# Kernel tuning notes

Hardware: AMD Instinct MI355X
Metric: run time of the kernel (lower is better)

The kernel has to match this reference:

```python
import jax, jax.numpy as jnp
import numpy as np

N = 2048        # reservoir_size
D_IN = 32       # input_dim
D_OUT = 16      # output_dim
H = 128         # PhysicsEncoder hidden_dim
B, T = 64, 256
LEAK = 0.3
CONNECTIVITY = 0.1
SPECTRAL_RADIUS = 0.95
LN_EPS = 1e-5


def setup_inputs() -> dict:
    key = jax.random.key(0)
    ks = jax.random.split(key, 24)
    x = jax.random.normal(ks[0], (B, T, D_IN), dtype=jnp.float32)
    # frozen input weights, input_scaling = 1.0
    W_in = jax.random.normal(ks[1], (N, D_IN), dtype=jnp.float32)
    # sparse reservoir, rescaled to spectral radius ~0.95 (analytic approx
    # rho ~ sigma*sqrt(N*p) for sparse gaussian, matches the torch rescale intent)
    mask = (jax.random.uniform(ks[2], (N, N)) < CONNECTIVITY).astype(jnp.float32)
    W_res = jax.random.normal(ks[3], (N, N), dtype=jnp.float32) * 0.1 * mask
    approx_radius = 0.1 * np.sqrt(N * CONNECTIVITY)
    W_res = W_res * (SPECTRAL_RADIUS / approx_radius)
    # attention: seq_len is always 1 inside the loop, so softmax over a length-1
    # axis is identically 1 and out == proj(v). Only the V slice of qkv matters.
    sc = 1.0 / np.sqrt(N)
    Wv = jax.random.uniform(ks[4], (N, N), minval=-sc, maxval=sc, dtype=jnp.float32)
    bv = jax.random.uniform(ks[5], (N,), minval=-sc, maxval=sc, dtype=jnp.float32)
    Wproj = jax.random.uniform(ks[6], (N, N), minval=-sc, maxval=sc, dtype=jnp.float32)
    bproj = jax.random.uniform(ks[7], (N,), minval=-sc, maxval=sc, dtype=jnp.float32)
    # physics encoder: Linear(N,H) -> LayerNorm -> GELU -> Linear(H,H) -> GELU -> Linear(H,N)
    s1 = 1.0 / np.sqrt(N)
    We1 = jax.random.uniform(ks[8], (H, N), minval=-s1, maxval=s1, dtype=jnp.float32)
    be1 = jax.random.uniform(ks[9], (H,), minval=-s1, maxval=s1, dtype=jnp.float32)
    ln_g = jnp.ones((H,), jnp.float32)
    ln_b = jnp.zeros((H,), jnp.float32)
    s2 = 1.0 / np.sqrt(H)
    We2 = jax.random.uniform(ks[10], (H, H), minval=-s2, maxval=s2, dtype=jnp.float32)
    be2 = jax.random.uniform(ks[11], (H,), minval=-s2, maxval=s2, dtype=jnp.float32)
    We3 = jax.random.uniform(ks[12], (N, H), minval=-s2, maxval=s2, dtype=jnp.float32)
    be3 = jax.random.uniform(ks[13], (N,), minval=-s2, maxval=s2, dtype=jnp.float32)
    # Bayesian output layer (reparameterized; epsilons passed in for determinism)
    s3 = 1.0 / np.sqrt(N)
    w_mu = jax.random.uniform(ks[14], (D_OUT, N), minval=-s3, maxval=s3, dtype=jnp.float32)
    w_rho = jnp.full((D_OUT, N), -3.0, jnp.float32)
    b_mu = jax.random.uniform(ks[15], (D_OUT,), minval=-s3, maxval=s3, dtype=jnp.float32)
    b_rho = jnp.full((D_OUT,), -3.0, jnp.float32)
    w_eps = jax.random.normal(ks[16], (D_OUT, N), dtype=jnp.float32)
    b_eps = jax.random.normal(ks[17], (D_OUT,), dtype=jnp.float32)
    return {
        "x": x, "W_in": W_in, "W_res": W_res,
        "Wv": Wv, "bv": bv, "Wproj": Wproj, "bproj": bproj,
        "We1": We1, "be1": be1, "ln_g": ln_g, "ln_b": ln_b,
        "We2": We2, "be2": be2, "We3": We3, "be3": be3,
        "w_mu": w_mu, "w_rho": w_rho, "b_mu": b_mu, "b_rho": b_rho,
        "w_eps": w_eps, "b_eps": b_eps,
    }


def _gelu(x):
    return jax.nn.gelu(x, approximate=False)  # torch nn.GELU default = exact erf


def reference(x, W_in, W_res, Wv, bv, Wproj, bproj,
              We1, be1, ln_g, ln_b, We2, be2, We3, be3,
              w_mu, w_rho, b_mu, b_rho, w_eps, b_eps):
    Bsz = x.shape[0]

    def step(states, x_t):
        # terms computed from PRE-attention state, as in the original loop order
        input_term = x_t @ W_in.T            # [B, N]
        reservoir_term = states @ W_res.T    # [B, N]
        # attention over a length-1 sequence: softmax == 1 -> out = proj(v)
        v = states @ Wv.T + bv
        s_att = v @ Wproj.T + bproj          # new `states` after attention
        # physics encoder on attended state
        h = s_att @ We1.T + be1
        mu = jnp.mean(h, axis=-1, keepdims=True)
        var = jnp.var(h, axis=-1, keepdims=True)
        h = (h - mu) * jax.lax.rsqrt(var + LN_EPS) * ln_g + ln_b
        h = _gelu(h)
        h = _gelu(h @ We2.T + be2)
        phys = h @ We3.T + be3               # [B, N]
        new_state = (1.0 - LEAK) * s_att + LEAK * jnp.tanh(
            input_term + reservoir_term + phys)
        return new_state, None

    s0 = jnp.zeros((Bsz, N), x.dtype)
    final_state, _ = jax.lax.scan(step, s0, jnp.swapaxes(x, 0, 1))  # scan over T

    # Bayesian output layer (reparameterization with fixed eps)
    w_sigma = jnp.log1p(jnp.exp(w_rho))
    b_sigma = jnp.log1p(jnp.exp(b_rho))
    weight = w_mu + w_sigma * w_eps
    bias = b_mu + b_sigma * b_eps
    predictions = final_state @ weight.T + bias  # [B, D_OUT]
    return predictions
```

## Files before the change

kernel.cpp:

```cpp
#include <hip/hip_runtime.h>
#include <hip/hip_fp16.h>
#include <cstdint>
#include <cstddef>

typedef _Float16 f16x8 __attribute__((ext_vector_type(8)));
typedef float    f32x4 __attribute__((ext_vector_type(4)));

#define MFMA(A,B,C) __builtin_amdgcn_mfma_f32_16x16x32_f16((A),(B),(C),0,0,0)

#define NRES  2048
#define DIN   32
#define DOUT  16
#define HDIM  128
#define BBATCH 64
#define TSTEPS 256
#define WCOLS 4224
#define NWORK 256
#define NBLK  257

#define OFF_WBIG  ((size_t)0)
#define OFF_WH1   ((size_t)16777216)
#define OFF_BIAS  ((size_t)17301504)
#define OFF_WE2H  ((size_t)17318400)
#define OFF_WE3H  ((size_t)17351168)
#define OFF_S16   ((size_t)17875456)
#define OFF_YP    ((size_t)18137600)
#define OFF_WINH  ((size_t)19219200)
#define OFF_CNT   ((size_t)19350528)

__device__ __forceinline__ float gelu_exact(float v) {
  return 0.5f * v * (1.0f + erff(v * 0.70710678118654752f));
}

__device__ __forceinline__ void stg16(void* p, f32x4 v) {
  asm volatile("global_store_dwordx4 %0, %1, off sc0 sc1" :: "v"(p), "v"(v) : "memory");
}


__global__ void k_cast(const float* __restrict__ src, _Float16* __restrict__ dst, int n) {
  int i = blockIdx.x * blockDim.x + threadIdx.x;
  int stride = gridDim.x * blockDim.x;
  for (; i < n; i += stride) dst[i] = (_Float16)src[i];
}

__global__ void k_batt(const float* __restrict__ Wproj, const float* __restrict__ bv,
                       const float* __restrict__ bproj, float* __restrict__ bias_big) {
  int c = blockIdx.x, tid = threadIdx.x;
  float p = 0.f;
  for (int k = tid; k < NRES; k += 256) p += Wproj[(size_t)c * NRES + k] * bv[k];
  for (int m = 1; m < 64; m <<= 1) p += __shfl_xor(p, m);
  __shared__ float r4[4];
  if ((tid & 63) == 0) r4[tid >> 6] = p;
  __syncthreads();
  if (tid == 0) bias_big[2048 + c] = r4[0] + r4[1] + r4[2] + r4[3] + bproj[c];
}

__global__ void k_bh1(const float* __restrict__ We1, const float* __restrict__ be1,
                      float* __restrict__ bias_big) {
  int h = blockIdx.x, tid = threadIdx.x;
  float p = 0.f;
  for (int n = tid; n < NRES; n += 256) p += We1[(size_t)h * NRES + n] * bias_big[2048 + n];
  for (int m = 1; m < 64; m <<= 1) p += __shfl_xor(p, m);
  __shared__ float r4[4];
  if ((tid & 63) == 0) r4[tid >> 6] = p;
  __syncthreads();
  if (tid == 0) bias_big[4096 + h] = r4[0] + r4[1] + r4[2] + r4[3] + be1[h];
}

__global__ void __launch_bounds__(256) k_gemm1(const float* __restrict__ Wproj,
                                               const float* __restrict__ Wv,
                                               _Float16* __restrict__ wbig) {
  __shared__ _Float16 BT[64][40];
  const int kblock = blockIdx.x, cblock = blockIdx.y;
  const int tid = threadIdx.x, wv = tid >> 6, lane = tid & 63;
  const int l4 = lane >> 4, l15 = lane & 15;
  const int crow0 = cblock * 64 + wv * 16;
  f32x4 acc[4];
  f32x4 zero = {0.f, 0.f, 0.f, 0.f};
  for (int i = 0; i < 4; ++i) acc[i] = zero;

  for (int mc = 0; mc < 64; ++mc) {
    const int m0 = mc * 32;
    {
      int m = tid >> 3, kk = (tid & 7) * 8;
      const float* src = &Wv[(size_t)(m0 + m) * NRES + kblock * 64 + kk];
      float4 v0 = *(const float4*)src;
      float4 v1 = *(const float4*)(src + 4);
      float tmp[8] = {v0.x, v0.y, v0.z, v0.w, v1.x, v1.y, v1.z, v1.w};
      #pragma unroll
      for (int j = 0; j < 8; ++j) BT[kk + j][m] = (_Float16)tmp[j];
    }
    __syncthreads();
    const float* pa = &Wproj[(size_t)(crow0 + l15) * NRES + m0 + l4 * 8];
    float4 a0 = *(const float4*)pa;
    float4 a1 = *(const float4*)(pa + 4);
    f16x8 af;
    af[0]=(_Float16)a0.x; af[1]=(_Float16)a0.y; af[2]=(_Float16)a0.z; af[3]=(_Float16)a0.w;
    af[4]=(_Float16)a1.x; af[5]=(_Float16)a1.y; af[6]=(_Float16)a1.z; af[7]=(_Float16)a1.w;
    #pragma unroll
    for (int kt = 0; kt < 4; ++kt) {
      f16x8 bf = *(const f16x8*)&BT[kt * 16 + l15][l4 * 8];
      acc[kt] = MFMA(af, bf, acc[kt]);
    }
    __syncthreads();
  }
  #pragma unroll
  for (int kt = 0; kt < 4; ++kt)
    #pragma unroll
    for (int i = 0; i < 4; ++i) {
      int c = crow0 + l4 * 4 + i;
      int k = kblock * 64 + kt * 16 + l15;
      wbig[(size_t)(2048 + c) * NRES + k] = (_Float16)acc[kt][i];
    }
}

__global__ void __launch_bounds__(256) k_gemm2(const float* __restrict__ We1,
                                               const _Float16* __restrict__ wbig,
                                               _Float16* __restrict__ wh1) {
  __shared__ _Float16 BT[64][40];
  const int kblock = blockIdx.x, hblock = blockIdx.y;
  const int tid = threadIdx.x, wv = tid >> 6, lane = tid & 63;
  const int l4 = lane >> 4, l15 = lane & 15;
  const int hrow0 = hblock * 64 + wv * 16;
  f32x4 acc[4];
  f32x4 zero = {0.f, 0.f, 0.f, 0.f};
  for (int i = 0; i < 4; ++i) acc[i] = zero;

  for (int nc = 0; nc < 64; ++nc) {
    const int n0 = nc * 32;
    {
      int n = tid >> 3, kk = (tid & 7) * 8;
      f16x8 v = *(const f16x8*)&wbig[(size_t)(2048 + n0 + n) * NRES + kblock * 64 + kk];
      #pragma unroll
      for (int j = 0; j < 8; ++j) BT[kk + j][n] = v[j];
    }
    __syncthreads();
    const float* pa = &We1[(size_t)(hrow0 + l15) * NRES + n0 + l4 * 8];
    float4 a0 = *(const float4*)pa;
    float4 a1 = *(const float4*)(pa + 4);
    f16x8 af;
    af[0]=(_Float16)a0.x; af[1]=(_Float16)a0.y; af[2]=(_Float16)a0.z; af[3]=(_Float16)a0.w;
    af[4]=(_Float16)a1.x; af[5]=(_Float16)a1.y; af[6]=(_Float16)a1.z; af[7]=(_Float16)a1.w;
    #pragma unroll
    for (int kt = 0; kt < 4; ++kt) {
      f16x8 bf = *(const f16x8*)&BT[kt * 16 + l15][l4 * 8];
      acc[kt] = MFMA(af, bf, acc[kt]);
    }
    __syncthreads();
  }
  #pragma unroll
  for (int kt = 0; kt < 4; ++kt)
    #pragma unroll
    for (int i = 0; i < 4; ++i) {
      int h = hrow0 + l4 * 4 + i;
      int k = kblock * 64 + kt * 16 + l15;
      wh1[(size_t)h * NRES + k] = (_Float16)acc[kt][i];
    }
}

__device__ __forceinline__ void gbar3(unsigned* slots, unsigned* wake, int b, unsigned phase) {
  asm volatile("s_waitcnt vmcnt(0)" ::: "memory");
  __syncthreads();
  if (threadIdx.x == 0) {
    __hip_atomic_store(slots + b, phase, __ATOMIC_RELAXED, __HIP_MEMORY_SCOPE_AGENT);
    unsigned spins = 0;
    while (__hip_atomic_load(wake + (size_t)b * 16, __ATOMIC_RELAXED, __HIP_MEMORY_SCOPE_AGENT) < phase) {
      __builtin_amdgcn_s_sleep(1);
      if (++spins > (1u << 20)) break;
    }
    (void)__hip_atomic_load(wake + (size_t)b * 16, __ATOMIC_ACQUIRE, __HIP_MEMORY_SCOPE_AGENT);
  }
  __syncthreads();
}


__global__ void __launch_bounds__(256, 2) k_main(
    const float* __restrict__ x,
    const float* __restrict__ ln_g, const float* __restrict__ ln_b,
    const float* __restrict__ be2v, const float* __restrict__ be3v,
    const float* __restrict__ w_mu, const float* __restrict__ w_rho,
    const float* __restrict__ b_mu, const float* __restrict__ b_rho,
    const float* __restrict__ w_eps, const float* __restrict__ b_eps,
    const _Float16* __restrict__ wbig, const _Float16* __restrict__ wh1,
    const float* __restrict__ bias_big,
    const _Float16* __restrict__ we2h, const _Float16* __restrict__ we3h,
    const _Float16* __restrict__ winh,
    _Float16* s16, float* yp,
    unsigned* cnt, float* __restrict__ out)
{
  const int b = blockIdx.x, tid = threadIdx.x;
  unsigned* slots = cnt;
  unsigned* wake  = cnt + 512;

  if (b == NWORK) {
    if (tid >= 64) return;
    for (unsigned p = 1; p <= 2u * TSTEPS; ++p) {
      unsigned spins = 0;
      for (;;) {
        bool ok = true;
        #pragma unroll
        for (int j = 0; j < 4; ++j) {
          unsigned v = __hip_atomic_load(slots + tid + j * 64, __ATOMIC_RELAXED, __HIP_MEMORY_SCOPE_AGENT);
          ok = ok && (v >= p);
        }
        if (__all((int)ok)) break;
        if (++spins > (1u << 19)) break;
        __builtin_amdgcn_s_sleep(1);
      }
      #pragma unroll
      for (int j = 0; j < 4; ++j)
        __hip_atomic_store(wake + (size_t)(tid + j * 64) * 16, p, __ATOMIC_RELAXED, __HIP_MEMORY_SCOPE_AGENT);
    }
    return;
  }

  const int wv = tid >> 6, lane = tid & 63;
  const int l4 = lane >> 4, l15 = lane & 15;

  __shared__ float    lds_red[4][64][17];
  __shared__ _Float16 lds_w2[128][136];
  __shared__ _Float16 lds_h1[16][136];
  __shared__ _Float16 lds_g2[16][136];
  __shared__ _Float16 lds_x[16][40];
  __shared__ _Float16 lds_ns[16][40];

  const bool dual = (b < 8);
  f16x8 Bf[16];
  #pragma unroll
  for (int ks = 0; ks < 16; ++ks)
    Bf[ks] = *(const f16x8*)&wbig[(size_t)(b * 16 + l15) * NRES + wv * 512 + ks * 32 + l4 * 8];
  const _Float16* wh1p = &wh1[(size_t)(b * 16 + l15) * NRES + wv * 512 + l4 * 8];

  const int R0 = (b >> 6) * 16, C0 = (b & 63) * 32;

  float g8[8], bb8[8], bh8[8];
  #pragma unroll
  for (int jj = 0; jj < 8; ++jj) {
    g8[jj]  = ln_g[l15 + 16 * jj];
    bb8[jj] = ln_b[l15 + 16 * jj];
    bh8[jj] = bias_big[4096 + l15 + 16 * jj];
  }
  float be2r[2];
  #pragma unroll
  for (int ct = 0; ct < 2; ++ct) be2r[ct] = be2v[(wv * 2 + ct) * 16 + l15];

  const int mycol = C0 + wv * 16 + l15;
  f16x8 We3f[4];
  f16x8 Winf;
  float be3r = 0.f, battr = 0.f;
  if (wv < 2) {
    #pragma unroll
    for (int ks = 0; ks < 4; ++ks)
      We3f[ks] = *(const f16x8*)&we3h[(size_t)mycol * HDIM + ks * 32 + l4 * 8];
    be3r  = be3v[mycol];
    battr = bias_big[2048 + mycol];
    Winf  = *(const f16x8*)&winh[(size_t)mycol * DIN + l4 * 8];
  }

  {
    int row = tid >> 1, half = tid & 1;
    #pragma unroll
    for (int j = 0; j < 8; ++j) {
      f16x8 v = *(const f16x8*)&we2h[(size_t)row * HDIM + half * 64 + j * 8];
      *(f16x8*)&lds_w2[row][half * 64 + j * 8] = v;
    }
  }
  __syncthreads();

  const f32x4 zero = {0.f, 0.f, 0.f, 0.f};
  unsigned phase = 0;

  const int cr  = tid >> 2, cch = tid & 3;
  const int rqi = (cr >> 4) * 4 + (cr & 3);
  const int pl4 = (cr >> 2) & 3;

  for (int t = 0; t < TSTEPS; ++t) {
    f32x4 a0 = zero, a1 = zero, a2 = zero, a3 = zero;
    f32x4 e0 = zero, e1 = zero, e2 = zero, e3 = zero;
    #pragma unroll
    for (int ks = 0; ks < 16; ++ks) {
      const int kk = wv * 512 + ks * 32 + l4 * 8;
      f16x8 A0 = *(const f16x8*)&s16[(size_t)(l15) * NRES + kk];
      f16x8 A1 = *(const f16x8*)&s16[(size_t)(16 + l15) * NRES + kk];
      f16x8 A2 = *(const f16x8*)&s16[(size_t)(32 + l15) * NRES + kk];
      f16x8 A3 = *(const f16x8*)&s16[(size_t)(48 + l15) * NRES + kk];
      a0 = MFMA(A0, Bf[ks], a0);
      a1 = MFMA(A1, Bf[ks], a1);
      a2 = MFMA(A2, Bf[ks], a2);
      a3 = MFMA(A3, Bf[ks], a3);
      if (dual) {
        f16x8 Bx = *(const f16x8*)&wh1p[ks * 32];
        e0 = MFMA(A0, Bx, e0);
        e1 = MFMA(A1, Bx, e1);
        e2 = MFMA(A2, Bx, e2);
        e3 = MFMA(A3, Bx, e3);
      }
    }
    #pragma unroll
    for (int i = 0; i < 4; ++i) {
      lds_red[wv][lane][0 + i]  = a0[i];
      lds_red[wv][lane][4 + i]  = a1[i];
      lds_red[wv][lane][8 + i]  = a2[i];
      lds_red[wv][lane][12 + i] = a3[i];
    }
    __syncthreads();
    {
      f32x4 v;
      #pragma unroll
      for (int c = 0; c < 4; ++c) {
        int pl = pl4 * 16 + cch * 4 + c;
        v[c] = lds_red[0][pl][rqi] + lds_red[1][pl][rqi]
             + lds_red[2][pl][rqi] + lds_red[3][pl][rqi];
      }
      stg16(&yp[(size_t)cr * WCOLS + b * 16 + cch * 4], v);
    }
    if (dual) {
      __syncthreads();
      #pragma unroll
      for (int i = 0; i < 4; ++i) {
        lds_red[wv][lane][0 + i]  = e0[i];
        lds_red[wv][lane][4 + i]  = e1[i];
        lds_red[wv][lane][8 + i]  = e2[i];
        lds_red[wv][lane][12 + i] = e3[i];
      }
      __syncthreads();
      f32x4 v2;
      #pragma unroll
      for (int c = 0; c < 4; ++c) {
        int pl = pl4 * 16 + cch * 4 + c;
        v2[c] = lds_red[0][pl][rqi] + lds_red[1][pl][rqi]
              + lds_red[2][pl][rqi] + lds_red[3][pl][rqi];
      }
      stg16(&yp[(size_t)cr * WCOLS + 4096 + b * 16 + cch * 4], v2);
    }
    ++phase;
    gbar3(slots, wake, b, phase);

    {
      int xr = tid >> 4, k0 = (tid & 15) * 2;
      const float* xs = &x[((size_t)(R0 + xr) * TSTEPS + t) * DIN + k0];
      lds_x[xr][k0]     = (_Float16)xs[0];
      lds_x[xr][k0 + 1] = (_Float16)xs[1];
    }
    const int lr = wv * 4 + l4;
    float h1v[8], s1 = 0.f, s2 = 0.f;
    const size_t yb = (size_t)(R0 + lr) * WCOLS + 4096;
    #pragma unroll
    for (int jj = 0; jj < 8; ++jj) {
      float v = yp[yb + l15 + 16 * jj] + bh8[jj];
      h1v[jj] = v; s1 += v; s2 += v * v;
    }
    #pragma unroll
    for (int m = 1; m < 16; m <<= 1) { s1 += __shfl_xor(s1, m); s2 += __shfl_xor(s2, m); }
    const float mu = s1 * (1.f / 128.f);
    const float var = s2 * (1.f / 128.f) - mu * mu;
    const float rs = rsqrtf(var + 1e-5f);
    #pragma unroll
    for (int jj = 0; jj < 8; ++jj) {
      float hn = (h1v[jj] - mu) * rs * g8[jj] + bb8[jj];
      lds_h1[lr][l15 + 16 * jj] = (_Float16)gelu_exact(hn);
    }
    __syncthreads();
    f32x4 c0 = zero, c1 = zero;
    #pragma unroll
    for (int ks = 0; ks < 4; ++ks) {
      f16x8 af = *(const f16x8*)&lds_h1[l15][ks * 32 + l4 * 8];
      f16x8 b0 = *(const f16x8*)&lds_w2[(wv * 2 + 0) * 16 + l15][ks * 32 + l4 * 8];
      f16x8 b1 = *(const f16x8*)&lds_w2[(wv * 2 + 1) * 16 + l15][ks * 32 + l4 * 8];
      c0 = MFMA(af, b0, c0);
      c1 = MFMA(af, b1, c1);
    }
    #pragma unroll
    for (int i = 0; i < 4; ++i) {
      int rr = l4 * 4 + i;
      lds_g2[rr][(wv * 2 + 0) * 16 + l15] = (_Float16)gelu_exact(c0[i] + be2r[0]);
      lds_g2[rr][(wv * 2 + 1) * 16 + l15] = (_Float16)gelu_exact(c1[i] + be2r[1]);
    }
    __syncthreads();
    if (wv < 2) {
      f32x4 accp = zero;
      #pragma unroll
      for (int ks = 0; ks < 4; ++ks) {
        f16x8 af = *(const f16x8*)&lds_g2[l15][ks * 32 + l4 * 8];
        accp = MFMA(af, We3f[ks], accp);
      }
      f16x8 ax = *(const f16x8*)&lds_x[l15][l4 * 8];
      f32x4 acci = MFMA(ax, Winf, zero);
      #pragma unroll
      for (int i = 0; i < 4; ++i) {
        int r2 = l4 * 4 + i;
        float satt = yp[(size_t)(R0 + r2) * WCOLS + 2048 + mycol] + battr;
        float rrv  = yp[(size_t)(R0 + r2) * WCOLS + mycol];
        float ns = 0.7f * satt + 0.3f * tanhf(acci[i] + rrv + accp[i] + be3r);
        lds_ns[r2][wv * 16 + l15] = (_Float16)ns;
      }
    }
    __syncthreads();
    if (tid < 64) {
      int r = tid >> 2, ch = tid & 3;
      f16x8 v = *(const f16x8*)&lds_ns[r][ch * 8];
      stg16(&s16[(size_t)(R0 + r) * NRES + C0 + ch * 8], __builtin_bit_cast(f32x4, v));
    }
    ++phase;
    gbar3(slots, wake, b, phase);
  }

  if (b < BBATCH) {
    float* red = &lds_red[0][0][0];
    int o = tid >> 4, sg = tid & 15;
    float p = 0.f;
    for (int n = sg * 128; n < sg * 128 + 128; ++n) {
      float sv = (float)s16[(size_t)b * NRES + n];
      float w = w_mu[(size_t)o * NRES + n]
              + log1pf(expf(w_rho[(size_t)o * NRES + n])) * w_eps[(size_t)o * NRES + n];
      p += sv * w;
    }
    red[o * 17 + sg] = p;
    __syncthreads();
    if (tid < DOUT) {
      float sum = 0.f;
      for (int q = 0; q < 16; ++q) sum += red[tid * 17 + q];
      float bs = b_mu[tid] + log1pf(expf(b_rho[tid])) * b_eps[tid];
      out[b * DOUT + tid] = sum + bs;
    }
  }
}


extern "C" void kernel_launch(void* const* d_in, const int* in_sizes, int n_in,
                              void* d_out, int out_size, void* d_ws, size_t ws_size,
                              hipStream_t stream) {
  (void)in_sizes; (void)n_in; (void)out_size; (void)ws_size;
  const float* x     = (const float*)d_in[0];
  const float* W_in  = (const float*)d_in[1];
  const float* W_res = (const float*)d_in[2];
  const float* Wv    = (const float*)d_in[3];
  const float* bv    = (const float*)d_in[4];
  const float* Wproj = (const float*)d_in[5];
  const float* bproj = (const float*)d_in[6];
  const float* We1   = (const float*)d_in[7];
  const float* be1   = (const float*)d_in[8];
  const float* ln_g  = (const float*)d_in[9];
  const float* ln_b  = (const float*)d_in[10];
  const float* We2   = (const float*)d_in[11];
  const float* be2   = (const float*)d_in[12];
  const float* We3   = (const float*)d_in[13];
  const float* be3   = (const float*)d_in[14];
  const float* w_mu  = (const float*)d_in[15];
  const float* w_rho = (const float*)d_in[16];
  const float* b_mu  = (const float*)d_in[17];
  const float* b_rho = (const float*)d_in[18];
  const float* w_eps = (const float*)d_in[19];
  const float* b_eps = (const float*)d_in[20];
  float* out = (float*)d_out;

  char* ws = (char*)d_ws;
  _Float16* wbig     = (_Float16*)(ws + OFF_WBIG);
  _Float16* wh1      = (_Float16*)(ws + OFF_WH1);
  float*    bias_big = (float*)(ws + OFF_BIAS);
  _Float16* we2h     = (_Float16*)(ws + OFF_WE2H);
  _Float16* we3h     = (_Float16*)(ws + OFF_WE3H);
  _Float16* s16      = (_Float16*)(ws + OFF_S16);
  float*    yp       = (float*)(ws + OFF_YP);
  _Float16* winh     = (_Float16*)(ws + OFF_WINH);
  unsigned* cnt      = (unsigned*)(ws + OFF_CNT);

  hipMemsetAsync(bias_big, 0, WCOLS * sizeof(float), stream);
  hipMemsetAsync(s16, 0, (size_t)BBATCH * NRES * sizeof(_Float16), stream);
  hipMemsetAsync(cnt, 0, 512 * 4 + 256 * 64, stream);

  k_cast<<<4096, 256, 0, stream>>>(W_res, wbig, NRES * NRES);
  k_cast<<<64,   256, 0, stream>>>(We2, we2h, HDIM * HDIM);
  k_cast<<<1024, 256, 0, stream>>>(We3, we3h, NRES * HDIM);
  k_cast<<<256,  256, 0, stream>>>(W_in, winh, NRES * DIN);
  k_batt<<<NRES, 256, 0, stream>>>(Wproj, bv, bproj, bias_big);
  k_gemm1<<<dim3(32, 32), 256, 0, stream>>>(Wproj, Wv, wbig);
  k_bh1<<<HDIM, 256, 0, stream>>>(We1, be1, bias_big);
  k_gemm2<<<dim3(32, 2), 256, 0, stream>>>(We1, wbig, wh1);

  k_main<<<NBLK, 256, 0, stream>>>(x, ln_g, ln_b, be2, be3,
                                   w_mu, w_rho, b_mu, b_rho, w_eps, b_eps,
                                   wbig, wh1, bias_big, we2h, we3h, winh, s16, yp, cnt, out);
}
```

Measured before the change: 6.630 ms.

## Software-pipeline state loads with cache-bypassing asm and move small weights to LDS

The per-step GEMV now loads the shared state through inline-asm global loads with sc0 sc1 bits, kept in a three-deep register ring with explicit vmcnt waits so loads overlap the MFMAs. The second weight tile (wh1) for the dual blocks is preloaded into registers instead of being re-read from global memory every step. The We3, W_in and layernorm parameters move from registers into LDS, and the acquire load in the barrier is removed, with the explicit coherent loads relied on instead. This aims to hide global latency in the serialized recurrence, at the cost of higher register pressure and memory-ordering subtleties around the removed acquire.

After: 7.984 ms. 1.2x slower.

```diff
diff --git a/kernel.cpp b/kernel.cpp
--- a/kernel.cpp
+++ b/kernel.cpp
@@ -35,6 +35,10 @@
 __device__ __forceinline__ void stg16(void* p, f32x4 v) {
   asm volatile("global_store_dwordx4 %0, %1, off sc0 sc1" :: "v"(p), "v"(v) : "memory");
 }
+#define LDG16(dst, ptr) \
+  asm volatile("global_load_dwordx4 %0, %1, off sc0 sc1" : "=v"(dst) : "v"(ptr) : "memory")
+#define LDGF(dst, ptr) \
+  asm volatile("global_load_dword %0, %1, off sc0 sc1" : "=v"(dst) : "v"(ptr) : "memory")
 
 
 __global__ void k_cast(const float* __restrict__ src, _Float16* __restrict__ dst, int n) {
@@ -168,7 +172,6 @@
       __builtin_amdgcn_s_sleep(1);
       if (++spins > (1u << 20)) break;
     }
-    (void)__hip_atomic_load(wake + (size_t)b * 16, __ATOMIC_ACQUIRE, __HIP_MEMORY_SCOPE_AGENT);
   }
   __syncthreads();
 }
@@ -219,53 +222,64 @@
 
   __shared__ float    lds_red[4][64][17];
   __shared__ _Float16 lds_w2[128][136];
+  __shared__ _Float16 lds_w3[32][136];
+  __shared__ _Float16 lds_wi[32][40];
+  __shared__ float    lds_lnp[3][128];
   __shared__ _Float16 lds_h1[16][136];
   __shared__ _Float16 lds_g2[16][136];
   __shared__ _Float16 lds_x[16][40];
   __shared__ _Float16 lds_ns[16][40];
 
   const bool dual = (b < 8);
-  f16x8 Bf[16];
+  f16x8 Bf[16], Bf2[16];
   #pragma unroll
   for (int ks = 0; ks < 16; ++ks)
     Bf[ks] = *(const f16x8*)&wbig[(size_t)(b * 16 + l15) * NRES + wv * 512 + ks * 32 + l4 * 8];
-  const _Float16* wh1p = &wh1[(size_t)(b * 16 + l15) * NRES + wv * 512 + l4 * 8];
+  if (dual) {
+    #pragma unroll
+    for (int ks = 0; ks < 16; ++ks)
+      Bf2[ks] = *(const f16x8*)&wh1[(size_t)(b * 16 + l15) * NRES + wv * 512 + ks * 32 + l4 * 8];
+  }
 
   const int R0 = (b >> 6) * 16, C0 = (b & 63) * 32;
-
-  float g8[8], bb8[8], bh8[8];
-  #pragma unroll
-  for (int jj = 0; jj < 8; ++jj) {
-    g8[jj]  = ln_g[l15 + 16 * jj];
-    bb8[jj] = ln_b[l15 + 16 * jj];
-    bh8[jj] = bias_big[4096 + l15 + 16 * jj];
-  }
+  const int mycol = C0 + wv * 16 + l15;
+  const int lcol  = wv * 16 + l15;
+
   float be2r[2];
   #pragma unroll
   for (int ct = 0; ct < 2; ++ct) be2r[ct] = be2v[(wv * 2 + ct) * 16 + l15];
-
-  const int mycol = C0 + wv * 16 + l15;
-  f16x8 We3f[4];
-  f16x8 Winf;
   float be3r = 0.f, battr = 0.f;
   if (wv < 2) {
-    #pragma unroll
-    for (int ks = 0; ks < 4; ++ks)
-      We3f[ks] = *(const f16x8*)&we3h[(size_t)mycol * HDIM + ks * 32 + l4 * 8];
     be3r  = be3v[mycol];
     battr = bias_big[2048 + mycol];
-    Winf  = *(const f16x8*)&winh[(size_t)mycol * DIN + l4 * 8];
   }
 
   {
     int row = tid >> 1, half = tid & 1;
     #pragma unroll
-    for (int j = 0; j < 8; ++j) {
-      f16x8 v = *(const f16x8*)&we2h[(size_t)row * HDIM + half * 64 + j * 8];
-      *(f16x8*)&lds_w2[row][half * 64 + j * 8] = v;
+    for (int j = 0; j < 8; ++j)
+      *(f16x8*)&lds_w2[row][half * 64 + j * 8] =
+          *(const f16x8*)&we2h[(size_t)row * HDIM + half * 64 + j * 8];
+    for (int idx = tid; idx < 32 * 16; idx += 256) {
+      int c = idx >> 4, kk8 = (idx & 15) * 8;
+      *(f16x8*)&lds_w3[c][kk8] = *(const f16x8*)&we3h[(size_t)(C0 + c) * HDIM + kk8];
+    }
+    for (int idx = tid; idx < 32 * 4; idx += 256) {
+      int c = idx >> 2, kk8 = (idx & 3) * 8;
+      *(f16x8*)&lds_wi[c][kk8] = *(const f16x8*)&winh[(size_t)(C0 + c) * DIN + kk8];
+    }
+    if (tid < 128) {
+      lds_lnp[0][tid] = ln_g[tid];
+      lds_lnp[1][tid] = ln_b[tid];
+      lds_lnp[2][tid] = bias_big[4096 + tid];
     }
   }
   __syncthreads();
+
+  const _Float16* q0 = s16 + (size_t)(l15) * NRES + wv * 512 + l4 * 8;
+  const _Float16* q1 = q0 + 16 * NRES;
+  const _Float16* q2 = q0 + 32 * NRES;
+  const _Float16* q3 = q0 + 48 * NRES;
 
   const f32x4 zero = {0.f, 0.f, 0.f, 0.f};
   unsigned phase = 0;
@@ -277,23 +291,38 @@
   for (int t = 0; t < TSTEPS; ++t) {
     f32x4 a0 = zero, a1 = zero, a2 = zero, a3 = zero;
     f32x4 e0 = zero, e1 = zero, e2 = zero, e3 = zero;
-    #pragma unroll
-    for (int ks = 0; ks < 16; ++ks) {
-      const int kk = wv * 512 + ks * 32 + l4 * 8;
-      f16x8 A0 = *(const f16x8*)&s16[(size_t)(l15) * NRES + kk];
-      f16x8 A1 = *(const f16x8*)&s16[(size_t)(16 + l15) * NRES + kk];
-      f16x8 A2 = *(const f16x8*)&s16[(size_t)(32 + l15) * NRES + kk];
-      f16x8 A3 = *(const f16x8*)&s16[(size_t)(48 + l15) * NRES + kk];
-      a0 = MFMA(A0, Bf[ks], a0);
-      a1 = MFMA(A1, Bf[ks], a1);
-      a2 = MFMA(A2, Bf[ks], a2);
-      a3 = MFMA(A3, Bf[ks], a3);
-      if (dual) {
-        f16x8 Bx = *(const f16x8*)&wh1p[ks * 32];
-        e0 = MFMA(A0, Bx, e0);
-        e1 = MFMA(A1, Bx, e1);
-        e2 = MFMA(A2, Bx, e2);
-        e3 = MFMA(A3, Bx, e3);
+    {
+      f16x8 A[3][4];
+      #pragma unroll
+      for (int c = 0; c < 3; ++c) {
+        LDG16(A[c][0], q0 + c * 32);
+        LDG16(A[c][1], q1 + c * 32);
+        LDG16(A[c][2], q2 + c * 32);
+        LDG16(A[c][3], q3 + c * 32);
+      }
+      #pragma unroll
+      for (int ks = 0; ks < 16; ++ks) {
+        if (ks <= 13)      { asm volatile("s_waitcnt vmcnt(8)" ::: "memory"); }
+        else if (ks == 14) { asm volatile("s_waitcnt vmcnt(4)" ::: "memory"); }
+        else               { asm volatile("s_waitcnt vmcnt(0)" ::: "memory"); }
+        __builtin_amdgcn_sched_barrier(0);
+        const int sl = ks % 3;
+        a0 = MFMA(A[sl][0], Bf[ks], a0);
+        a1 = MFMA(A[sl][1], Bf[ks], a1);
+        a2 = MFMA(A[sl][2], Bf[ks], a2);
+        a3 = MFMA(A[sl][3], Bf[ks], a3);
+        if (dual) {
+          e0 = MFMA(A[sl][0], Bf2[ks], e0);
+          e1 = MFMA(A[sl][1], Bf2[ks], e1);
+          e2 = MFMA(A[sl][2], Bf2[ks], e2);
+          e3 = MFMA(A[sl][3], Bf2[ks], e3);
+        }
+        if (ks + 3 < 16) {
+          LDG16(A[sl][0], q0 + (ks + 3) * 32);
+          LDG16(A[sl][1], q1 + (ks + 3) * 32);
+          LDG16(A[sl][2], q2 + (ks + 3) * 32);
+          LDG16(A[sl][3], q3 + (ks + 3) * 32);
+        }
       }
     }
     #pragma unroll
@@ -343,11 +372,18 @@
       lds_x[xr][k0 + 1] = (_Float16)xs[1];
     }
     const int lr = wv * 4 + l4;
+    float hv[8];
+    {
+      const float* hp = &yp[(size_t)(R0 + lr) * WCOLS + 4096 + l15];
+      #pragma unroll
+      for (int jj = 0; jj < 8; ++jj) LDGF(hv[jj], hp + 16 * jj);
+      asm volatile("s_waitcnt vmcnt(0)" ::: "memory");
+      __builtin_amdgcn_sched_barrier(0);
+    }
     float h1v[8], s1 = 0.f, s2 = 0.f;
-    const size_t yb = (size_t)(R0 + lr) * WCOLS + 4096;
     #pragma unroll
     for (int jj = 0; jj < 8; ++jj) {
-      float v = yp[yb + l15 + 16 * jj] + bh8[jj];
+      float v = hv[jj] + lds_lnp[2][l15 + 16 * jj];
       h1v[jj] = v; s1 += v; s2 += v * v;
     }
     #pragma unroll
@@ -357,8 +393,9 @@
     const float rs = rsqrtf(var + 1e-5f);
     #pragma unroll
     for (int jj = 0; jj < 8; ++jj) {
-      float hn = (h1v[jj] - mu) * rs * g8[jj] + bb8[jj];
-      lds_h1[lr][l15 + 16 * jj] = (_Float16)gelu_exact(hn);
+      int j = l15 + 16 * jj;
+      float hn = (h1v[jj] - mu) * rs * lds_lnp[0][j] + lds_lnp[1][j];
+      lds_h1[lr][j] = (_Float16)gelu_exact(hn);
     }
     __syncthreads();
     f32x4 c0 = zero, c1 = zero;
@@ -378,20 +415,31 @@
     }
     __syncthreads();
     if (wv < 2) {
+      float sattv[4], rrvv[4];
+      #pragma unroll
+      for (int i = 0; i < 4; ++i) {
+        const float* pa_ = &yp[(size_t)(R0 + l4 * 4 + i) * WCOLS + 2048 + mycol];
+        const float* pb_ = &yp[(size_t)(R0 + l4 * 4 + i) * WCOLS + mycol];
+        LDGF(sattv[i], pa_);
+        LDGF(rrvv[i], pb_);
+      }
       f32x4 accp = zero;
       #pragma unroll
       for (int ks = 0; ks < 4; ++ks) {
         f16x8 af = *(const f16x8*)&lds_g2[l15][ks * 32 + l4 * 8];
-        accp = MFMA(af, We3f[ks], accp);
+        f16x8 w3 = *(const f16x8*)&lds_w3[lcol][ks * 32 + l4 * 8];
+        accp = MFMA(af, w3, accp);
       }
       f16x8 ax = *(const f16x8*)&lds_x[l15][l4 * 8];
-      f32x4 acci = MFMA(ax, Winf, zero);
+      f16x8 wi = *(const f16x8*)&lds_wi[lcol][l4 * 8];
+      f32x4 acci = MFMA(ax, wi, zero);
+      asm volatile("s_waitcnt vmcnt(0)" ::: "memory");
+      __builtin_amdgcn_sched_barrier(0);
       #pragma unroll
       for (int i = 0; i < 4; ++i) {
         int r2 = l4 * 4 + i;
-        float satt = yp[(size_t)(R0 + r2) * WCOLS + 2048 + mycol] + battr;
-        float rrv  = yp[(size_t)(R0 + r2) * WCOLS + mycol];
-        float ns = 0.7f * satt + 0.3f * tanhf(acci[i] + rrv + accp[i] + be3r);
+        float satt = sattv[i] + battr;
+        float ns = 0.7f * satt + 0.3f * tanhf(acci[i] + rrvv[i] + accp[i] + be3r);
         lds_ns[r2][wv * 16 + l15] = (_Float16)ns;
       }
     }
@@ -408,12 +456,25 @@
   if (b < BBATCH) {
     float* red = &lds_red[0][0][0];
     int o = tid >> 4, sg = tid & 15;
+    f16x8 sbuf[16];
+    {
+      const _Float16* sp = &s16[(size_t)b * NRES + sg * 128];
+      #pragma unroll
+      for (int jj = 0; jj < 16; ++jj) LDG16(sbuf[jj], sp + jj * 8);
+      asm volatile("s_waitcnt vmcnt(0)" ::: "memory");
+      __builtin_amdgcn_sched_barrier(0);
+    }
     float p = 0.f;
-    for (int n = sg * 128; n < sg * 128 + 128; ++n) {
-      float sv = (float)s16[(size_t)b * NRES + n];
-      float w = w_mu[(size_t)o * NRES + n]
-              + log1pf(expf(w_rho[(size_t)o * NRES + n])) * w_eps[(size_t)o * NRES + n];
-      p += sv * w;
+    #pragma unroll
+    for (int jj = 0; jj < 16; ++jj) {
+      #pragma unroll
+      for (int k = 0; k < 8; ++k) {
+        int n = sg * 128 + jj * 8 + k;
+        float sv = (float)sbuf[jj][k];
+        float w = w_mu[(size_t)o * NRES + n]
+                + log1pf(expf(w_rho[(size_t)o * NRES + n])) * w_eps[(size_t)o * NRES + n];
+        p += sv * w;
+      }
     }
     red[o * 17 + sg] = p;
     __syncthreads();
```

## Interleave reservoir and attention weight rows to halve grid barriers per step

Applied to the files above, without the earlier changes.

W_res and the fused Wproj·Wv rows are packed so each block's 16 output columns hold 8 reservoir and the matching 8 attention columns. This lets every block finish its own state update locally without the yp global scratch exchange. The encoder first layer moves to 4 dedicated blocks that work on a double-buffered state and signal through per-block flags. The result is one grid barrier per timestep instead of two. The trade-off is that the encoder blocks carry extra serial work that every block must wait on, and half the MFMA output lanes in the final step are wasted.

After: 9.719 ms. +46.6%, slower.

```diff
diff --git a/kernel.cpp b/kernel.cpp
--- a/kernel.cpp
+++ b/kernel.cpp
@@ -14,19 +14,19 @@
 #define HDIM  128
 #define BBATCH 64
 #define TSTEPS 256
-#define WCOLS 4224
 #define NWORK 256
 #define NBLK  257
-
-#define OFF_WBIG  ((size_t)0)
+#define S16N  (BBATCH * NRES)
+
+#define OFF_WPK   ((size_t)0)
 #define OFF_WH1   ((size_t)16777216)
 #define OFF_BIAS  ((size_t)17301504)
 #define OFF_WE2H  ((size_t)17318400)
 #define OFF_WE3H  ((size_t)17351168)
 #define OFF_S16   ((size_t)17875456)
-#define OFF_YP    ((size_t)18137600)
-#define OFF_WINH  ((size_t)19219200)
-#define OFF_CNT   ((size_t)19350528)
+#define OFF_WINH  ((size_t)18399744)
+#define OFF_G2    ((size_t)18530816)
+#define OFF_CNT   ((size_t)18547200)
 
 __device__ __forceinline__ float gelu_exact(float v) {
   return 0.5f * v * (1.0f + erff(v * 0.70710678118654752f));
@@ -41,6 +41,15 @@
   int i = blockIdx.x * blockDim.x + threadIdx.x;
   int stride = gridDim.x * blockDim.x;
   for (; i < n; i += stride) dst[i] = (_Float16)src[i];
+}
+
+__global__ void k_castres(const float* __restrict__ W_res, _Float16* __restrict__ wpk) {
+  int c = blockIdx.x, k0 = threadIdx.x * 8;
+  int pr = (c >> 3) * 16 + (c & 7);
+  const float* s = &W_res[(size_t)c * NRES + k0];
+  _Float16* d = &wpk[(size_t)pr * NRES + k0];
+  #pragma unroll
+  for (int j = 0; j < 8; ++j) d[j] = (_Float16)s[j];
 }
 
 __global__ void k_batt(const float* __restrict__ Wproj, const float* __restrict__ bv,
@@ -69,7 +78,7 @@
 
 __global__ void __launch_bounds__(256) k_gemm1(const float* __restrict__ Wproj,
                                                const float* __restrict__ Wv,
-                                               _Float16* __restrict__ wbig) {
+                                               _Float16* __restrict__ wpk) {
   __shared__ _Float16 BT[64][40];
   const int kblock = blockIdx.x, cblock = blockIdx.y;
   const int tid = threadIdx.x, wv = tid >> 6, lane = tid & 63;
@@ -110,12 +119,13 @@
     for (int i = 0; i < 4; ++i) {
       int c = crow0 + l4 * 4 + i;
       int k = kblock * 64 + kt * 16 + l15;
-      wbig[(size_t)(2048 + c) * NRES + k] = (_Float16)acc[kt][i];
+      int pr = (c >> 3) * 16 + 8 + (c & 7);
+      wpk[(size_t)pr * NRES + k] = (_Float16)acc[kt][i];
     }
 }
 
 __global__ void __launch_bounds__(256) k_gemm2(const float* __restrict__ We1,
-                                               const _Float16* __restrict__ wbig,
+                                               const _Float16* __restrict__ wpk,
                                                _Float16* __restrict__ wh1) {
   __shared__ _Float16 BT[64][40];
   const int kblock = blockIdx.x, hblock = blockIdx.y;
@@ -130,7 +140,9 @@
     const int n0 = nc * 32;
     {
       int n = tid >> 3, kk = (tid & 7) * 8;
-      f16x8 v = *(const f16x8*)&wbig[(size_t)(2048 + n0 + n) * NRES + kblock * 64 + kk];
+      int nn = n0 + n;
+      int pr = (nn >> 3) * 16 + 8 + (nn & 7);
+      f16x8 v = *(const f16x8*)&wpk[(size_t)pr * NRES + kblock * 64 + kk];
       #pragma unroll
       for (int j = 0; j < 8; ++j) BT[kk + j][n] = v[j];
     }
@@ -181,20 +193,21 @@
     const float* __restrict__ w_mu, const float* __restrict__ w_rho,
     const float* __restrict__ b_mu, const float* __restrict__ b_rho,
     const float* __restrict__ w_eps, const float* __restrict__ b_eps,
-    const _Float16* __restrict__ wbig, const _Float16* __restrict__ wh1,
+    const _Float16* __restrict__ wpk, const _Float16* __restrict__ wh1,
     const float* __restrict__ bias_big,
     const _Float16* __restrict__ we2h, const _Float16* __restrict__ we3h,
     const _Float16* __restrict__ winh,
-    _Float16* s16, float* yp,
+    _Float16* s16, _Float16* g2buf,
     unsigned* cnt, float* __restrict__ out)
 {
   const int b = blockIdx.x, tid = threadIdx.x;
-  unsigned* slots = cnt;
+  unsigned* fg2   = cnt;
+  unsigned* slots = cnt + 64;
   unsigned* wake  = cnt + 512;
 
   if (b == NWORK) {
     if (tid >= 64) return;
-    for (unsigned p = 1; p <= 2u * TSTEPS; ++p) {
+    for (unsigned p = 1; p <= (unsigned)TSTEPS; ++p) {
       unsigned spins = 0;
       for (;;) {
         bool ok = true;
@@ -220,82 +233,169 @@
   __shared__ float    lds_red[4][64][17];
   __shared__ _Float16 lds_w2[128][136];
   __shared__ _Float16 lds_h1[16][136];
-  __shared__ _Float16 lds_g2[16][136];
-  __shared__ _Float16 lds_x[16][40];
-  __shared__ _Float16 lds_ns[16][40];
-
-  const bool dual = (b < 8);
+  __shared__ _Float16 lds_x[64][40];
+  __shared__ _Float16 lds_ns[64][16];
+
+  const bool hduty = (b < 4);
+  const int  hrt   = b;
+
   f16x8 Bf[16];
   #pragma unroll
   for (int ks = 0; ks < 16; ++ks)
-    Bf[ks] = *(const f16x8*)&wbig[(size_t)(b * 16 + l15) * NRES + wv * 512 + ks * 32 + l4 * 8];
-  const _Float16* wh1p = &wh1[(size_t)(b * 16 + l15) * NRES + wv * 512 + l4 * 8];
-
-  const int R0 = (b >> 6) * 16, C0 = (b & 63) * 32;
-
-  float g8[8], bb8[8], bh8[8];
-  #pragma unroll
-  for (int jj = 0; jj < 8; ++jj) {
-    g8[jj]  = ln_g[l15 + 16 * jj];
-    bb8[jj] = ln_b[l15 + 16 * jj];
-    bh8[jj] = bias_big[4096 + l15 + 16 * jj];
-  }
-  float be2r[2];
-  #pragma unroll
-  for (int ct = 0; ct < 2; ++ct) be2r[ct] = be2v[(wv * 2 + ct) * 16 + l15];
-
-  const int mycol = C0 + wv * 16 + l15;
+    Bf[ks] = *(const f16x8*)&wpk[(size_t)(b * 16 + l15) * NRES + wv * 512 + ks * 32 + l4 * 8];
+
+  const int mycol = 8 * b + (l15 & 7);
+  const bool colv = (l15 < 8);
+  f16x8 zf;
+  #pragma unroll
+  for (int j = 0; j < 8; ++j) zf[j] = (_Float16)0.f;
   f16x8 We3f[4];
-  f16x8 Winf;
-  float be3r = 0.f, battr = 0.f;
-  if (wv < 2) {
+  f16x8 Winf = zf;
+  if (colv) {
     #pragma unroll
     for (int ks = 0; ks < 4; ++ks)
       We3f[ks] = *(const f16x8*)&we3h[(size_t)mycol * HDIM + ks * 32 + l4 * 8];
-    be3r  = be3v[mycol];
-    battr = bias_big[2048 + mycol];
-    Winf  = *(const f16x8*)&winh[(size_t)mycol * DIN + l4 * 8];
-  }
+    Winf = *(const f16x8*)&winh[(size_t)mycol * DIN + l4 * 8];
+  } else {
+    #pragma unroll
+    for (int ks = 0; ks < 4; ++ks) We3f[ks] = zf;
+  }
+  const float be3r  = colv ? be3v[mycol] : 0.f;
+  const float battr = colv ? bias_big[2048 + mycol] : 0.f;
+
+  float g8[8], bb8[8], bh8[8];
+  #pragma unroll
+  for (int ct = 0; ct < 8; ++ct) {
+    g8[ct]  = ln_g[ct * 16 + l15];
+    bb8[ct] = ln_b[ct * 16 + l15];
+    bh8[ct] = bias_big[4096 + ct * 16 + l15];
+  }
+  float be2r[2];
+  #pragma unroll
+  for (int ct = 0; ct < 2; ++ct) be2r[ct] = be2v[(wv * 2 + ct) * 16 + l15];
 
   {
     int row = tid >> 1, half = tid & 1;
     #pragma unroll
-    for (int j = 0; j < 8; ++j) {
-      f16x8 v = *(const f16x8*)&we2h[(size_t)row * HDIM + half * 64 + j * 8];
-      *(f16x8*)&lds_w2[row][half * 64 + j * 8] = v;
-    }
+    for (int j = 0; j < 8; ++j)
+      *(f16x8*)&lds_w2[row][half * 64 + j * 8] =
+          *(const f16x8*)&we2h[(size_t)row * HDIM + half * 64 + j * 8];
   }
   __syncthreads();
 
   const f32x4 zero = {0.f, 0.f, 0.f, 0.f};
-  unsigned phase = 0;
-
-  const int cr  = tid >> 2, cch = tid & 3;
-  const int rqi = (cr >> 4) * 4 + (cr & 3);
-  const int pl4 = (cr >> 2) & 3;
+  const int laneR = (l4 << 4) | (l15 & 7);
+  const int laneA = laneR + 8;
 
   for (int t = 0; t < TSTEPS; ++t) {
+    const _Float16* sread = s16 + (size_t)(t & 1) * S16N;
+    _Float16* swrite      = s16 + (size_t)((t + 1) & 1) * S16N;
+
+    if (hduty) {
+      f32x4 hacc[8];
+      #pragma unroll
+      for (int ct = 0; ct < 8; ++ct) hacc[ct] = zero;
+      for (int kc = 0; kc < 16; ++kc) {
+        f16x8 Ah = *(const f16x8*)&sread[(size_t)(hrt * 16 + l15) * NRES + wv * 512 + kc * 32 + l4 * 8];
+        #pragma unroll
+        for (int ct = 0; ct < 8; ++ct) {
+          f16x8 Bh = *(const f16x8*)&wh1[(size_t)(ct * 16 + l15) * NRES + wv * 512 + kc * 32 + l4 * 8];
+          hacc[ct] = MFMA(Ah, Bh, hacc[ct]);
+        }
+      }
+      float hv[32];
+      #pragma unroll
+      for (int ct = 0; ct < 4; ++ct)
+        #pragma unroll
+        for (int i = 0; i < 4; ++i) lds_red[wv][lane][ct * 4 + i] = hacc[ct][i];
+      __syncthreads();
+      #pragma unroll
+      for (int ct = 0; ct < 4; ++ct)
+        #pragma unroll
+        for (int i = 0; i < 4; ++i)
+          hv[ct * 4 + i] = lds_red[0][lane][ct * 4 + i] + lds_red[1][lane][ct * 4 + i]
+                         + lds_red[2][lane][ct * 4 + i] + lds_red[3][lane][ct * 4 + i];
+      __syncthreads();
+      #pragma unroll
+      for (int ct = 0; ct < 4; ++ct)
+        #pragma unroll
+        for (int i = 0; i < 4; ++i) lds_red[wv][lane][ct * 4 + i] = hacc[4 + ct][i];
+      __syncthreads();
+      #pragma unroll
+      for (int ct = 4; ct < 8; ++ct)
+        #pragma unroll
+        for (int i = 0; i < 4; ++i)
+          hv[ct * 4 + i] = lds_red[0][lane][(ct - 4) * 4 + i] + lds_red[1][lane][(ct - 4) * 4 + i]
+                         + lds_red[2][lane][(ct - 4) * 4 + i] + lds_red[3][lane][(ct - 4) * 4 + i];
+      __syncthreads();
+      float s1v[4] = {0.f, 0.f, 0.f, 0.f}, s2v[4] = {0.f, 0.f, 0.f, 0.f};
+      #pragma unroll
+      for (int ct = 0; ct < 8; ++ct)
+        #pragma unroll
+        for (int i = 0; i < 4; ++i) {
+          float v = hv[ct * 4 + i] + bh8[ct];
+          hv[ct * 4 + i] = v; s1v[i] += v; s2v[i] += v * v;
+        }
+      #pragma unroll
+      for (int m = 1; m < 16; m <<= 1)
+        #pragma unroll
+        for (int i = 0; i < 4; ++i) { s1v[i] += __shfl_xor(s1v[i], m); s2v[i] += __shfl_xor(s2v[i], m); }
+      #pragma unroll
+      for (int i = 0; i < 4; ++i) {
+        float mu = s1v[i] * (1.f / 128.f);
+        float var = s2v[i] * (1.f / 128.f) - mu * mu;
+        float rs = rsqrtf(var + 1e-5f);
+        if (wv == 0) {
+          #pragma unroll
+          for (int ct = 0; ct < 8; ++ct) {
+            float hn = (hv[ct * 4 + i] - mu) * rs * g8[ct] + bb8[ct];
+            lds_h1[l4 * 4 + i][ct * 16 + l15] = (_Float16)gelu_exact(hn);
+          }
+        }
+      }
+      __syncthreads();
+      f32x4 c0 = zero, c1 = zero;
+      #pragma unroll
+      for (int ks = 0; ks < 4; ++ks) {
+        f16x8 af = *(const f16x8*)&lds_h1[l15][ks * 32 + l4 * 8];
+        f16x8 b0 = *(const f16x8*)&lds_w2[(wv * 2 + 0) * 16 + l15][ks * 32 + l4 * 8];
+        f16x8 b1 = *(const f16x8*)&lds_w2[(wv * 2 + 1) * 16 + l15][ks * 32 + l4 * 8];
+        c0 = MFMA(af, b0, c0);
+        c1 = MFMA(af, b1, c1);
+      }
+      __syncthreads();
+      #pragma unroll
+      for (int i = 0; i < 4; ++i) {
+        int rr = l4 * 4 + i;
+        lds_h1[rr][(wv * 2 + 0) * 16 + l15] = (_Float16)gelu_exact(c0[i] + be2r[0]);
+        lds_h1[rr][(wv * 2 + 1) * 16 + l15] = (_Float16)gelu_exact(c1[i] + be2r[1]);
+      }
+      __syncthreads();
+      {
+        int row = tid >> 4, ch = tid & 15;
+        f16x8 v = *(const f16x8*)&lds_h1[row][ch * 8];
+        stg16(&g2buf[(size_t)(hrt * 16 + row) * HDIM + ch * 8], __builtin_bit_cast(f32x4, v));
+      }
+      asm volatile("s_waitcnt vmcnt(0)" ::: "memory");
+      __syncthreads();
+      if (tid == 0)
+        __hip_atomic_store(fg2 + hrt, (unsigned)(t + 1), __ATOMIC_RELAXED, __HIP_MEMORY_SCOPE_AGENT);
+    }
+
     f32x4 a0 = zero, a1 = zero, a2 = zero, a3 = zero;
-    f32x4 e0 = zero, e1 = zero, e2 = zero, e3 = zero;
     #pragma unroll
     for (int ks = 0; ks < 16; ++ks) {
       const int kk = wv * 512 + ks * 32 + l4 * 8;
-      f16x8 A0 = *(const f16x8*)&s16[(size_t)(l15) * NRES + kk];
-      f16x8 A1 = *(const f16x8*)&s16[(size_t)(16 + l15) * NRES + kk];
-      f16x8 A2 = *(const f16x8*)&s16[(size_t)(32 + l15) * NRES + kk];
-      f16x8 A3 = *(const f16x8*)&s16[(size_t)(48 + l15) * NRES + kk];
+      f16x8 A0 = *(const f16x8*)&sread[(size_t)(l15) * NRES + kk];
+      f16x8 A1 = *(const f16x8*)&sread[(size_t)(16 + l15) * NRES + kk];
+      f16x8 A2 = *(const f16x8*)&sread[(size_t)(32 + l15) * NRES + kk];
+      f16x8 A3 = *(const f16x8*)&sread[(size_t)(48 + l15) * NRES + kk];
       a0 = MFMA(A0, Bf[ks], a0);
       a1 = MFMA(A1, Bf[ks], a1);
       a2 = MFMA(A2, Bf[ks], a2);
       a3 = MFMA(A3, Bf[ks], a3);
-      if (dual) {
-        f16x8 Bx = *(const f16x8*)&wh1p[ks * 32];
-        e0 = MFMA(A0, Bx, e0);
-        e1 = MFMA(A1, Bx, e1);
-        e2 = MFMA(A2, Bx, e2);
-        e3 = MFMA(A3, Bx, e3);
-      }
-    }
+    }
+    __syncthreads();
     #pragma unroll
     for (int i = 0; i < 4; ++i) {
       lds_red[wv][lane][0 + i]  = a0[i];
@@ -303,106 +403,58 @@
       lds_red[wv][lane][8 + i]  = a2[i];
       lds_red[wv][lane][12 + i] = a3[i];
     }
-    __syncthreads();
     {
-      f32x4 v;
-      #pragma unroll
-      for (int c = 0; c < 4; ++c) {
-        int pl = pl4 * 16 + cch * 4 + c;
-        v[c] = lds_red[0][pl][rqi] + lds_red[1][pl][rqi]
-             + lds_red[2][pl][rqi] + lds_red[3][pl][rqi];
-      }
-      stg16(&yp[(size_t)cr * WCOLS + b * 16 + cch * 4], v);
-    }
-    if (dual) {
-      __syncthreads();
+      int row = tid >> 2, k0 = (tid & 3) * 8;
+      const float* xs = &x[((size_t)row * TSTEPS + t) * DIN + k0];
+      float4 v0 = *(const float4*)xs;
+      float4 v1 = *(const float4*)(xs + 4);
+      _Float16* d = &lds_x[row][k0];
+      d[0]=(_Float16)v0.x; d[1]=(_Float16)v0.y; d[2]=(_Float16)v0.z; d[3]=(_Float16)v0.w;
+      d[4]=(_Float16)v1.x; d[5]=(_Float16)v1.y; d[6]=(_Float16)v1.z; d[7]=(_Float16)v1.w;
+    }
+    if (tid == 0) {
+      unsigned spins = 0;
+      for (;;) {
+        unsigned mn = 0xFFFFFFFFu;
+        #pragma unroll
+        for (int j = 0; j < 4; ++j) {
+          unsigned v = __hip_atomic_load(fg2 + j, __ATOMIC_RELAXED, __HIP_MEMORY_SCOPE_AGENT);
+          mn = v < mn ? v : mn;
+        }
+        if (mn >= (unsigned)(t + 1)) break;
+        __builtin_amdgcn_s_sleep(1);
+        if (++spins > (1u << 20)) break;
+      }
+      (void)__hip_atomic_load(fg2, __ATOMIC_ACQUIRE, __HIP_MEMORY_SCOPE_AGENT);
+    }
+    __syncthreads();
+
+    {
+      f32x4 accp = zero;
+      #pragma unroll
+      for (int kc = 0; kc < 4; ++kc) {
+        f16x8 ag = *(const f16x8*)&g2buf[(size_t)(wv * 16 + l15) * HDIM + kc * 32 + l4 * 8];
+        accp = MFMA(ag, We3f[kc], accp);
+      }
+      f16x8 ax = *(const f16x8*)&lds_x[wv * 16 + l15][l4 * 8];
+      f32x4 acci = MFMA(ax, Winf, zero);
       #pragma unroll
       for (int i = 0; i < 4; ++i) {
-        lds_red[wv][lane][0 + i]  = e0[i];
-        lds_red[wv][lane][4 + i]  = e1[i];
-        lds_red[wv][lane][8 + i]  = e2[i];
-        lds_red[wv][lane][12 + i] = e3[i];
-      }
-      __syncthreads();
-      f32x4 v2;
-      #pragma unroll
-      for (int c = 0; c < 4; ++c) {
-        int pl = pl4 * 16 + cch * 4 + c;
-        v2[c] = lds_red[0][pl][rqi] + lds_red[1][pl][rqi]
-              + lds_red[2][pl][rqi] + lds_red[3][pl][rqi];
-      }
-      stg16(&yp[(size_t)cr * WCOLS + 4096 + b * 16 + cch * 4], v2);
-    }
-    ++phase;
-    gbar3(slots, wake, b, phase);
-
-    {
-      int xr = tid >> 4, k0 = (tid & 15) * 2;
-      const float* xs = &x[((size_t)(R0 + xr) * TSTEPS + t) * DIN + k0];
-      lds_x[xr][k0]     = (_Float16)xs[0];
-      lds_x[xr][k0 + 1] = (_Float16)xs[1];
-    }
-    const int lr = wv * 4 + l4;
-    float h1v[8], s1 = 0.f, s2 = 0.f;
-    const size_t yb = (size_t)(R0 + lr) * WCOLS + 4096;
-    #pragma unroll
-    for (int jj = 0; jj < 8; ++jj) {
-      float v = yp[yb + l15 + 16 * jj] + bh8[jj];
-      h1v[jj] = v; s1 += v; s2 += v * v;
-    }
-    #pragma unroll
-    for (int m = 1; m < 16; m <<= 1) { s1 += __shfl_xor(s1, m); s2 += __shfl_xor(s2, m); }
-    const float mu = s1 * (1.f / 128.f);
-    const float var = s2 * (1.f / 128.f) - mu * mu;
-    const float rs = rsqrtf(var + 1e-5f);
-    #pragma unroll
-    for (int jj = 0; jj < 8; ++jj) {
-      float hn = (h1v[jj] - mu) * rs * g8[jj] + bb8[jj];
-      lds_h1[lr][l15 + 16 * jj] = (_Float16)gelu_exact(hn);
-    }
-    __syncthreads();
-    f32x4 c0 = zero, c1 = zero;
-    #pragma unroll
-    for (int ks = 0; ks < 4; ++ks) {
-      f16x8 af = *(const f16x8*)&lds_h1[l15][ks * 32 + l4 * 8];
-      f16x8 b0 = *(const f16x8*)&lds_w2[(wv * 2 + 0) * 16 + l15][ks * 32 + l4 * 8];
-      f16x8 b1 = *(const f16x8*)&lds_w2[(wv * 2 + 1) * 16 + l15][ks * 32 + l4 * 8];
-      c0 = MFMA(af, b0, c0);
-      c1 = MFMA(af, b1, c1);
-    }
-    #pragma unroll
-    for (int i = 0; i < 4; ++i) {
-      int rr = l4 * 4 + i;
-      lds_g2[rr][(wv * 2 + 0) * 16 + l15] = (_Float16)gelu_exact(c0[i] + be2r[0]);
-      lds_g2[rr][(wv * 2 + 1) * 16 + l15] = (_Float16)gelu_exact(c1[i] + be2r[1]);
-    }
-    __syncthreads();
-    if (wv < 2) {
-      f32x4 accp = zero;
-      #pragma unroll
-      for (int ks = 0; ks < 4; ++ks) {
-        f16x8 af = *(const f16x8*)&lds_g2[l15][ks * 32 + l4 * 8];
-        accp = MFMA(af, We3f[ks], accp);
-      }
-      f16x8 ax = *(const f16x8*)&lds_x[l15][l4 * 8];
-      f32x4 acci = MFMA(ax, Winf, zero);
-      #pragma unroll
-      for (int i = 0; i < 4; ++i) {
-        int r2 = l4 * 4 + i;
-        float satt = yp[(size_t)(R0 + r2) * WCOLS + 2048 + mycol] + battr;
-        float rrv  = yp[(size_t)(R0 + r2) * WCOLS + mycol];
-        float ns = 0.7f * satt + 0.3f * tanhf(acci[i] + rrv + accp[i] + be3r);
-        lds_ns[r2][wv * 16 + l15] = (_Float16)ns;
+        float rr = lds_red[0][laneR][wv * 4 + i] + lds_red[1][laneR][wv * 4 + i]
+                 + lds_red[2][laneR][wv * 4 + i] + lds_red[3][laneR][wv * 4 + i];
+        float sa = lds_red[0][laneA][wv * 4 + i] + lds_red[1][laneA][wv * 4 + i]
+                 + lds_red[2][laneA][wv * 4 + i] + lds_red[3][laneA][wv * 4 + i];
+        float ns = 0.7f * (sa + battr) + 0.3f * tanhf(acci[i] + rr + accp[i] + be3r);
+        if (colv) lds_ns[wv * 16 + l4 * 4 + i][l15] = (_Float16)ns;
       }
     }
     __syncthreads();
     if (tid < 64) {
-      int r = tid >> 2, ch = tid & 3;
-      f16x8 v = *(const f16x8*)&lds_ns[r][ch * 8];
-      stg16(&s16[(size_t)(R0 + r) * NRES + C0 + ch * 8], __builtin_bit_cast(f32x4, v));
-    }
-    ++phase;
-    gbar3(slots, wake, b, phase);
+      f16x8 v = *(const f16x8*)&lds_ns[tid][0];
+      stg16(&swrite[(size_t)tid * NRES + 8 * b], __builtin_bit_cast(f32x4, v));
+    }
+
+    gbar3(slots, wake, b, (unsigned)(t + 1));
   }
 
   if (b < BBATCH) {
@@ -455,30 +507,31 @@
   float* out = (float*)d_out;
 
   char* ws = (char*)d_ws;
-  _Float16* wbig     = (_Float16*)(ws + OFF_WBIG);
+  _Float16* wpk      = (_Float16*)(ws + OFF_WPK);
   _Float16* wh1      = (_Float16*)(ws + OFF_WH1);
   float*    bias_big = (float*)(ws + OFF_BIAS);
   _Float16* we2h     = (_Float16*)(ws + OFF_WE2H);
   _Float16* we3h     = (_Float16*)(ws + OFF_WE3H);
   _Float16* s16      = (_Float16*)(ws + OFF_S16);
-  float*    yp       = (float*)(ws + OFF_YP);
   _Float16* winh     = (_Float16*)(ws + OFF_WINH);
+  _Float16* g2buf    = (_Float16*)(ws + OFF_G2);
   unsigned* cnt      = (unsigned*)(ws + OFF_CNT);
 
-  hipMemsetAsync(bias_big, 0, WCOLS * sizeof(float), stream);
-  hipMemsetAsync(s16, 0, (size_t)BBATCH * NRES * sizeof(_Float16), stream);
-  hipMemsetAsync(cnt, 0, 512 * 4 + 256 * 64, stream);
-
-  k_cast<<<4096, 256, 0, stream>>>(W_res, wbig, NRES * NRES);
+  hipMemsetAsync(bias_big, 0, 4224 * sizeof(float), stream);
+  hipMemsetAsync(s16, 0, 2 * (size_t)S16N * sizeof(_Float16), stream);
+  hipMemsetAsync(cnt, 0, (512 + 4096) * 4, stream);
+
+  k_castres<<<2048, 256, 0, stream>>>(W_res, wpk);
   k_cast<<<64,   256, 0, stream>>>(We2, we2h, HDIM * HDIM);
   k_cast<<<1024, 256, 0, stream>>>(We3, we3h, NRES * HDIM);
   k_cast<<<256,  256, 0, stream>>>(W_in, winh, NRES * DIN);
   k_batt<<<NRES, 256, 0, stream>>>(Wproj, bv, bproj, bias_big);
-  k_gemm1<<<dim3(32, 32), 256, 0, stream>>>(Wproj, Wv, wbig);
+  k_gemm1<<<dim3(32, 32), 256, 0, stream>>>(Wproj, Wv, wpk);
   k_bh1<<<HDIM, 256, 0, stream>>>(We1, be1, bias_big);
-  k_gemm2<<<dim3(32, 2), 256, 0, stream>>>(We1, wbig, wh1);
+  k_gemm2<<<dim3(32, 2), 256, 0, stream>>>(We1, wpk, wh1);
 
   k_main<<<NBLK, 256, 0, stream>>>(x, ln_g, ln_b, be2, be3,
                                    w_mu, w_rho, b_mu, b_rho, w_eps, b_eps,
-                                   wbig, wh1, bias_big, we2h, we3h, winh, s16, yp, cnt, out);
-}
+                                   wpk, wh1, bias_big, we2h, we3h, winh,
+                                   s16, g2buf, cnt, out);
+}
```
